# Kernel optimization log

Measured on AMD Instinct MI355X. Metric: run time of the kernel, lower is better.

Reference implementation:

```python
import jax, jax.numpy as jnp
import numpy as np

# Mamba hyperparams derived from DRMamba.__init__: d_model=dim=96, d_state=16, d_conv=4, expand=2
D_MODEL = 96
D_INNER = 192          # expand * d_model
D_STATE = 16
D_CONV = 4
DT_RANK = 6            # ceil(d_model / 16)
REVERSE = True


def setup_inputs() -> dict:
    key = jax.random.key(0)
    ks = jax.random.split(key, 8)
    s = lambda k, shape: jax.random.normal(k, shape, jnp.float32) * 0.02
    x = jax.random.normal(ks[0], (8, 96, 64, 64), jnp.float32)
    in_proj_w = s(ks[1], (2 * D_INNER, D_MODEL))
    conv_w = s(ks[2], (D_INNER, 1, D_CONV))            # depthwise conv kernel (O, I/groups=1, K)
    conv_b = jnp.zeros((D_INNER,), jnp.float32)
    x_proj_w = s(ks[3], (DT_RANK + 2 * D_STATE, D_INNER))
    dt_proj_w = s(ks[4], (D_INNER, DT_RANK))
    dt_proj_b = s(ks[5], (D_INNER,))
    # S4D-real init, as in standard Mamba
    A_log = jnp.log(jnp.broadcast_to(jnp.arange(1, D_STATE + 1, dtype=jnp.float32), (D_INNER, D_STATE)))
    D = jnp.ones((D_INNER,), jnp.float32)
    out_proj_w = s(ks[6], (D_MODEL, D_INNER))
    return dict(x=x, in_proj_w=in_proj_w, conv_w=conv_w, conv_b=conv_b,
                x_proj_w=x_proj_w, dt_proj_w=dt_proj_w, dt_proj_b=dt_proj_b,
                A_log=A_log, D=D, out_proj_w=out_proj_w)


def reference(x, in_proj_w, conv_w, conv_b, x_proj_w, dt_proj_w, dt_proj_b, A_log, D, out_proj_w):
    b, c, h, w = x.shape
    xs = jnp.flip(x, 1) if REVERSE else x
    seq = xs.reshape(b, c, h * w).transpose(0, 2, 1)              # (b, l, d_model)
    xz = seq @ in_proj_w.T                                        # (b, l, 2*d_inner)
    u, res = jnp.split(xz, 2, axis=-1)
    # causal depthwise conv1d over sequence (torch: padding=d_conv-1 then truncate to l)
    uc = jax.lax.conv_general_dilated(
        u.transpose(0, 2, 1), conv_w, (1,), [(D_CONV - 1, 0)],
        dimension_numbers=('NCH', 'OIH', 'NCH'), feature_group_count=D_INNER)
    uc = uc + conv_b[None, :, None]
    u = jax.nn.silu(uc.transpose(0, 2, 1))                        # (b, l, d_inner)
    # input-dependent SSM parameters
    dbc = u @ x_proj_w.T                                          # (b, l, dt_rank + 2*d_state)
    dt, B, C = jnp.split(dbc, [DT_RANK, DT_RANK + D_STATE], axis=-1)
    delta = jax.nn.softplus(dt @ dt_proj_w.T + dt_proj_b)         # (b, l, d_inner)
    A = -jnp.exp(A_log)                                           # (d_inner, d_state)
    dA = jnp.exp(jnp.einsum('bld,dn->bldn', delta, A))            # discretized A
    dBu = jnp.einsum('bld,bln,bld->bldn', delta, B, u)            # discretized B * u

    def step(state, inp):
        dA_t, dBu_t, C_t = inp                                    # (b,d,n), (b,d,n), (b,n)
        state = dA_t * state + dBu_t
        y_t = jnp.einsum('bdn,bn->bd', state, C_t)
        return state, y_t

    init = jnp.zeros((b, D_INNER, D_STATE), u.dtype)
    _, ys = jax.lax.scan(step, init,
                         (dA.transpose(1, 0, 2, 3), dBu.transpose(1, 0, 2, 3), C.transpose(1, 0, 2)))
    y = ys.transpose(1, 0, 2) + u * D                             # (b, l, d_inner)
    y = y * jax.nn.silu(res)
    out = y @ out_proj_w.T                                        # (b, l, d_model)
    out = out.transpose(0, 2, 1).reshape(b, c, h, w)
    return jnp.flip(out, 1) if REVERSE else out
```

## Files before the change

kernel.cpp:

```cpp
#include <hip/hip_runtime.h>
#include <math.h>

#define NBATCH 8
#define SEQL   4096
#define DMODEL 96
#define DINNER 192
#define DSTATE 16
#define NDBC   38
#define NCHUNK 128
#define CSTEP  32

__device__ __forceinline__ float siluf(float x) {
    return x / (1.f + expf(-x));
}
__device__ __forceinline__ float softplusf(float x) {
    return (x > 20.f) ? x : log1pf(expf(x));
}

__global__ __launch_bounds__(128) void k_in_proj(const float* __restrict__ x,
                                                 const float* __restrict__ w,
                                                 float* __restrict__ u_raw,
                                                 float* __restrict__ res)
{
    __shared__ float As[32][128];
    __shared__ float Wt[32][68];
    const int tid = threadIdx.x;
    const int jg = tid & 7;
    const int lg = tid >> 3;
    const int b = blockIdx.z;
    const int l0 = blockIdx.x * 128;
    const int jb = blockIdx.y * 64;

    float acc[8][8];
#pragma unroll
    for (int r = 0; r < 8; r++)
#pragma unroll
        for (int c = 0; c < 8; c++) acc[r][c] = 0.f;

    for (int kb = 0; kb < 3; kb++) {
        {
            const int ll4 = tid & 31;
            const int m0 = tid >> 5;
#pragma unroll
            for (int i = 0; i < 8; i++) {
                const int m = m0 + 4 * i;
                const float4 v = *reinterpret_cast<const float4*>(
                    &x[((size_t)b * 96 + (95 - (kb * 32 + m))) * 4096 + l0 + ll4 * 4]);
                *reinterpret_cast<float4*>(&As[m][ll4 * 4]) = v;
            }
        }
        {
            const int k4 = tid & 7;
            const int jl0 = tid >> 3;
#pragma unroll
            for (int i = 0; i < 4; i++) {
                const int jl = jl0 + 16 * i;
                const float4 v = *reinterpret_cast<const float4*>(
                    &w[(size_t)(jb + jl) * 96 + kb * 32 + k4 * 4]);
                Wt[k4 * 4 + 0][jl] = v.x;
                Wt[k4 * 4 + 1][jl] = v.y;
                Wt[k4 * 4 + 2][jl] = v.z;
                Wt[k4 * 4 + 3][jl] = v.w;
            }
        }
        __syncthreads();
#pragma unroll
        for (int k = 0; k < 32; k++) {
            const float4 a0 = *reinterpret_cast<const float4*>(&As[k][lg * 8]);
            const float4 a1 = *reinterpret_cast<const float4*>(&As[k][lg * 8 + 4]);
            const float4 w0 = *reinterpret_cast<const float4*>(&Wt[k][jg * 8]);
            const float4 w1 = *reinterpret_cast<const float4*>(&Wt[k][jg * 8 + 4]);
            const float av[8] = {a0.x, a0.y, a0.z, a0.w, a1.x, a1.y, a1.z, a1.w};
            const float wv[8] = {w0.x, w0.y, w0.z, w0.w, w1.x, w1.y, w1.z, w1.w};
#pragma unroll
            for (int r = 0; r < 8; r++)
#pragma unroll
                for (int c = 0; c < 8; c++) acc[r][c] = fmaf(av[r], wv[c], acc[r][c]);
        }
        __syncthreads();
    }

    float* outp;
    int col0;
    if (jb < 192) { outp = u_raw; col0 = jb + jg * 8; }
    else          { outp = res;   col0 = jb - 192 + jg * 8; }
#pragma unroll
    for (int r = 0; r < 8; r++) {
        const int row = l0 + lg * 8 + r;
        float* rowp = &outp[((size_t)b * 4096 + row) * 192 + col0];
        *reinterpret_cast<float4*>(rowp) =
            make_float4(acc[r][0], acc[r][1], acc[r][2], acc[r][3]);
        *reinterpret_cast<float4*>(rowp + 4) =
            make_float4(acc[r][4], acc[r][5], acc[r][6], acc[r][7]);
    }
}

__global__ __launch_bounds__(256) void k_xproj(const float* __restrict__ u_raw,
                                               const float* __restrict__ w,
                                               const float* __restrict__ cw,
                                               const float* __restrict__ cb,
                                               float* __restrict__ u,
                                               float* __restrict__ dbc,
                                               float* __restrict__ Barr,
                                               float* __restrict__ Carr)
{
    __shared__ float Ur[67][33];
    __shared__ float Us[64][36];
    __shared__ float Ws[64 * 32];
    const int tid = threadIdx.x, tx = tid & 15, ty = tid >> 4;
    const int b = blockIdx.y;
    const int l0 = blockIdx.x * 64;

    float acc[4][4];
#pragma unroll
    for (int r = 0; r < 4; r++)
#pragma unroll
        for (int c = 0; c < 4; c++) acc[r][c] = 0.f;

    const int ch = tid & 31;
    const int lblk = tid >> 5;

    for (int kb = 0; kb < 6; kb++) {
        for (int idx = tid; idx < 536; idx += 256) {
            const int row = idx >> 3;
            const int c4 = idx & 7;
            const int gl = l0 - 3 + row;
            float4 v = make_float4(0.f, 0.f, 0.f, 0.f);
            if (gl >= 0)
                v = *reinterpret_cast<const float4*>(
                    &u_raw[((size_t)b * 4096 + gl) * 192 + kb * 32 + c4 * 4]);
            Ur[row][c4 * 4 + 0] = v.x;
            Ur[row][c4 * 4 + 1] = v.y;
            Ur[row][c4 * 4 + 2] = v.z;
            Ur[row][c4 * 4 + 3] = v.w;
        }
        {
            const int k4 = tid & 7;
            const int jb0 = tid >> 3;
#pragma unroll
            for (int i = 0; i < 2; i++) {
                const int jl = jb0 + 32 * i;
                float4 v = make_float4(0.f, 0.f, 0.f, 0.f);
                if (jl < NDBC)
                    v = *reinterpret_cast<const float4*>(&w[(size_t)jl * 192 + kb * 32 + k4 * 4]);
                *reinterpret_cast<float4*>(
                    &Ws[jl * 32 + ((k4 ^ ((jl >> 2) & 7)) << 2)]) = v;
            }
        }
        __syncthreads();

        {
            const float4 wc = *reinterpret_cast<const float4*>(&cw[(kb * 32 + ch) * 4]);
            const float bias = cb[kb * 32 + ch];
#pragma unroll
            for (int r = 0; r < 8; r++) {
                const int l = lblk * 8 + r;
                float s = bias;
                s = fmaf(wc.x, Ur[l + 0][ch], s);
                s = fmaf(wc.y, Ur[l + 1][ch], s);
                s = fmaf(wc.z, Ur[l + 2][ch], s);
                s = fmaf(wc.w, Ur[l + 3][ch], s);
                Us[l][ch] = siluf(s);
            }
        }
        __syncthreads();

        for (int idx = tid; idx < 512; idx += 256) {
            const int row = idx >> 3;
            const int c4 = idx & 7;
            const float4 v = *reinterpret_cast<const float4*>(&Us[row][c4 * 4]);
            *reinterpret_cast<float4*>(
                &u[((size_t)b * 4096 + l0 + row) * 192 + kb * 32 + c4 * 4]) = v;
        }

        const int sw = tx & 7;
#pragma unroll
        for (int k4 = 0; k4 < 8; k4++) {
            float4 a4[4];
#pragma unroll
            for (int r = 0; r < 4; r++)
                a4[r] = *reinterpret_cast<const float4*>(&Us[ty * 4 + r][k4 * 4]);
            float4 w4[4];
#pragma unroll
            for (int c = 0; c < 4; c++)
                w4[c] = *reinterpret_cast<const float4*>(
                    &Ws[(tx * 4 + c) * 32 + ((k4 ^ sw) << 2)]);
#pragma unroll
            for (int r = 0; r < 4; r++)
#pragma unroll
                for (int c = 0; c < 4; c++) {
                    acc[r][c] = fmaf(a4[r].x, w4[c].x, acc[r][c]);
                    acc[r][c] = fmaf(a4[r].y, w4[c].y, acc[r][c]);
                    acc[r][c] = fmaf(a4[r].z, w4[c].z, acc[r][c]);
                    acc[r][c] = fmaf(a4[r].w, w4[c].w, acc[r][c]);
                }
        }
        __syncthreads();
    }

#pragma unroll
    for (int r = 0; r < 4; r++) {
        const size_t row = (size_t)b * 4096 + l0 + ty * 4 + r;
#pragma unroll
        for (int c = 0; c < 4; c++) {
            const int j = tx * 4 + c;
            if (j < 6)       dbc[row * NDBC + j] = acc[r][c];
            else if (j < 22) Barr[row * 16 + (j - 6)] = acc[r][c];
            else if (j < 38) Carr[row * 16 + (j - 22)] = acc[r][c];
        }
    }
}

__global__ __launch_bounds__(768) void k_dtproj(const float* __restrict__ dbc,
                                                const float* __restrict__ w,
                                                const float* __restrict__ bias,
                                                float* __restrict__ delta)
{
    const int j = threadIdx.x;
    const int row = blockIdx.x * 4 + threadIdx.y;
    const int b = blockIdx.y;
    const size_t g = (size_t)b * 4096 + row;
    const float* dr = &dbc[g * NDBC];
    float s = bias[j];
#pragma unroll
    for (int k = 0; k < 6; k++) s = fmaf(dr[k], w[j * 6 + k], s);
    delta[g * 192 + j] = softplusf(s);
}

__global__ __launch_bounds__(192) void k_scan1(const float* __restrict__ delta,
                                               const float* __restrict__ u,
                                               const float* __restrict__ Barr,
                                               const float* __restrict__ A_log,
                                               float* __restrict__ P,
                                               float* __restrict__ S)
{
    const int d = threadIdx.x;
    const int c = blockIdx.x;
    const int b = blockIdx.y;

    float a[16];
    {
        const float4* al = reinterpret_cast<const float4*>(&A_log[d * 16]);
#pragma unroll
        for (int i = 0; i < 4; i++) {
            const float4 v = al[i];
            a[4 * i + 0] = -expf(v.x);
            a[4 * i + 1] = -expf(v.y);
            a[4 * i + 2] = -expf(v.z);
            a[4 * i + 3] = -expf(v.w);
        }
    }
    float st[16], p[16];
#pragma unroll
    for (int n = 0; n < 16; n++) { st[n] = 0.f; p[n] = 1.f; }

    const size_t g0 = (size_t)b * 4096 + (size_t)c * CSTEP;
    const float* dp = delta + g0 * 192 + d;
    const float* up = u + g0 * 192 + d;
    const float* bp = Barr + g0 * 16;

#pragma unroll 2
    for (int t = 0; t < CSTEP; t++) {
        const float dt = dp[t * 192];
        const float dtu = dt * up[t * 192];
        float Bv[16];
        {
            const float4* b4 = reinterpret_cast<const float4*>(bp + t * 16);
#pragma unroll
            for (int i = 0; i < 4; i++) {
                const float4 v = b4[i];
                Bv[4 * i + 0] = v.x; Bv[4 * i + 1] = v.y;
                Bv[4 * i + 2] = v.z; Bv[4 * i + 3] = v.w;
            }
        }
#pragma unroll
        for (int n = 0; n < 16; n++) {
            const float dA = __expf(dt * a[n]);
            p[n] *= dA;
            st[n] = fmaf(dA, st[n], dtu * Bv[n]);
        }
    }

    const size_t idx = (((size_t)b * NCHUNK + c) * 192 + d) * 16;
    float4* Pp = reinterpret_cast<float4*>(&P[idx]);
    float4* Sp = reinterpret_cast<float4*>(&S[idx]);
#pragma unroll
    for (int i = 0; i < 4; i++) {
        Pp[i] = make_float4(p[4 * i], p[4 * i + 1], p[4 * i + 2], p[4 * i + 3]);
        Sp[i] = make_float4(st[4 * i], st[4 * i + 1], st[4 * i + 2], st[4 * i + 3]);
    }
}

__global__ __launch_bounds__(256) void k_scan2(const float* __restrict__ P,
                                               float* __restrict__ S)
{
    const int dn = blockIdx.x * 256 + threadIdx.x;
    const int b = blockIdx.y;
    float carry = 0.f;
    const size_t base = (size_t)b * NCHUNK * 3072 + dn;
#pragma unroll 8
    for (int c = 0; c < NCHUNK; c++) {
        const size_t idx = base + (size_t)c * 3072;
        const float p = P[idx];
        const float s = S[idx];
        S[idx] = carry;
        carry = fmaf(p, carry, s);
    }
}

__global__ __launch_bounds__(192) void k_scan3(const float* __restrict__ delta,
                                               const float* __restrict__ u,
                                               const float* __restrict__ Barr,
                                               const float* __restrict__ Carr,
                                               const float* __restrict__ A_log,
                                               const float* __restrict__ S,
                                               const float* __restrict__ Dp,
                                               const float* __restrict__ res,
                                               float* __restrict__ y)
{
    const int d = threadIdx.x;
    const int c = blockIdx.x;
    const int b = blockIdx.y;

    float a[16];
    {
        const float4* al = reinterpret_cast<const float4*>(&A_log[d * 16]);
#pragma unroll
        for (int i = 0; i < 4; i++) {
            const float4 v = al[i];
            a[4 * i + 0] = -expf(v.x);
            a[4 * i + 1] = -expf(v.y);
            a[4 * i + 2] = -expf(v.z);
            a[4 * i + 3] = -expf(v.w);
        }
    }
    float st[16];
    {
        const float4* Sp = reinterpret_cast<const float4*>(
            &S[(((size_t)b * NCHUNK + c) * 192 + d) * 16]);
#pragma unroll
        for (int i = 0; i < 4; i++) {
            const float4 v = Sp[i];
            st[4 * i + 0] = v.x; st[4 * i + 1] = v.y;
            st[4 * i + 2] = v.z; st[4 * i + 3] = v.w;
        }
    }
    const float Dd = Dp[d];

    const size_t g0 = (size_t)b * 4096 + (size_t)c * CSTEP;
    const float* dp = delta + g0 * 192 + d;
    const float* up = u + g0 * 192 + d;
    const float* rp = res + g0 * 192 + d;
    float* yp = y + g0 * 192 + d;
    const float* bp = Barr + g0 * 16;
    const float* cp = Carr + g0 * 16;

#pragma unroll 2
    for (int t = 0; t < CSTEP; t++) {
        const float dt = dp[t * 192];
        const float ut = up[t * 192];
        const float dtu = dt * ut;
        float Bv[16], Cv[16];
        {
            const float4* b4 = reinterpret_cast<const float4*>(bp + t * 16);
            const float4* c4 = reinterpret_cast<const float4*>(cp + t * 16);
#pragma unroll
            for (int i = 0; i < 4; i++) {
                const float4 v = b4[i];
                Bv[4 * i + 0] = v.x; Bv[4 * i + 1] = v.y;
                Bv[4 * i + 2] = v.z; Bv[4 * i + 3] = v.w;
                const float4 w = c4[i];
                Cv[4 * i + 0] = w.x; Cv[4 * i + 1] = w.y;
                Cv[4 * i + 2] = w.z; Cv[4 * i + 3] = w.w;
            }
        }
        float yt = 0.f;
#pragma unroll
        for (int n = 0; n < 16; n++) {
            const float dA = __expf(dt * a[n]);
            st[n] = fmaf(dA, st[n], dtu * Bv[n]);
            yt = fmaf(st[n], Cv[n], yt);
        }
        const float r = rp[t * 192];
        const float sig = __builtin_amdgcn_rcpf(1.f + __expf(-r));
        yp[t * 192] = fmaf(ut, Dd, yt) * (r * sig);
    }
}

__global__ __launch_bounds__(256) void k_outproj(const float* __restrict__ y,
                                                 const float* __restrict__ w,
                                                 float* __restrict__ out)
{
    __shared__ float Ws[64 * 32];
    const int tid = threadIdx.x, tx = tid & 15, ty = tid >> 4;
    const int b = blockIdx.z;
    const int l0 = blockIdx.x * 128;
    const int jb = blockIdx.y * 64;

    float acc[8][4];
#pragma unroll
    for (int r = 0; r < 8; r++)
#pragma unroll
        for (int c = 0; c < 4; c++) acc[r][c] = 0.f;

    for (int kb = 0; kb < 6; kb++) {
        {
            const int k4 = tid & 7;
            const int jb0 = tid >> 3;
#pragma unroll
            for (int i = 0; i < 2; i++) {
                const int jl = jb0 + 32 * i;
                const int j = jb + jl;
                float4 v = make_float4(0.f, 0.f, 0.f, 0.f);
                if (j < 96)
                    v = *reinterpret_cast<const float4*>(&w[(size_t)j * 192 + kb * 32 + k4 * 4]);
                *reinterpret_cast<float4*>(
                    &Ws[jl * 32 + ((k4 ^ ((jl >> 2) & 7)) << 2)]) = v;
            }
        }
        __syncthreads();
        const int sw = tx & 7;
#pragma unroll
        for (int k4 = 0; k4 < 8; k4++) {
            float4 a4[8];
#pragma unroll
            for (int r = 0; r < 8; r++) {
                const int row = l0 + ty * 8 + r;
                a4[r] = *reinterpret_cast<const float4*>(
                    &y[((size_t)b * 4096 + row) * 192 + kb * 32 + k4 * 4]);
            }
            float4 w4[4];
#pragma unroll
            for (int c = 0; c < 4; c++)
                w4[c] = *reinterpret_cast<const float4*>(
                    &Ws[(tx * 4 + c) * 32 + ((k4 ^ sw) << 2)]);
#pragma unroll
            for (int r = 0; r < 8; r++)
#pragma unroll
                for (int c = 0; c < 4; c++) {
                    acc[r][c] = fmaf(a4[r].x, w4[c].x, acc[r][c]);
                    acc[r][c] = fmaf(a4[r].y, w4[c].y, acc[r][c]);
                    acc[r][c] = fmaf(a4[r].z, w4[c].z, acc[r][c]);
                    acc[r][c] = fmaf(a4[r].w, w4[c].w, acc[r][c]);
                }
        }
        __syncthreads();
    }
#pragma unroll
    for (int c = 0; c < 4; c++) {
        const int j = jb + tx * 4 + c;
        if (j < 96) {
            const int ch = 95 - j;
            const float4 v0 = make_float4(acc[0][c], acc[1][c], acc[2][c], acc[3][c]);
            const float4 v1 = make_float4(acc[4][c], acc[5][c], acc[6][c], acc[7][c]);
            const size_t base = ((size_t)b * 96 + ch) * 4096 + l0 + ty * 8;
            *reinterpret_cast<float4*>(&out[base]) = v0;
            *reinterpret_cast<float4*>(&out[base + 4]) = v1;
        }
    }
}

extern "C" void kernel_launch(void* const* d_in, const int* in_sizes, int n_in,
                              void* d_out, int out_size, void* d_ws, size_t ws_size,
                              hipStream_t stream)
{
    const float* x       = (const float*)d_in[0];
    const float* in_w    = (const float*)d_in[1];
    const float* conv_w  = (const float*)d_in[2];
    const float* conv_b  = (const float*)d_in[3];
    const float* xproj_w = (const float*)d_in[4];
    const float* dt_w    = (const float*)d_in[5];
    const float* dt_b    = (const float*)d_in[6];
    const float* A_log   = (const float*)d_in[7];
    const float* Dp      = (const float*)d_in[8];
    const float* out_w   = (const float*)d_in[9];

    float* ws    = (float*)d_ws;
    float* u_raw = ws;
    float* res   = u_raw + 6291456;
    float* u     = res   + 6291456;
    float* delta = u     + 6291456;
    float* dbc   = delta + 6291456;
    float* Barr  = dbc   + 1245184;
    float* Carr  = Barr  + 524288;
    float* P     = Carr  + 524288;
    float* S     = P     + 3145728;
    float* yfin  = u_raw;

    hipLaunchKernelGGL(k_in_proj, dim3(32, 6, 8), dim3(128), 0, stream, x, in_w, u_raw, res);
    hipLaunchKernelGGL(k_xproj,   dim3(64, 8),    dim3(256), 0, stream,
                       u_raw, xproj_w, conv_w, conv_b, u, dbc, Barr, Carr);
    hipLaunchKernelGGL(k_dtproj,  dim3(1024, 8),  dim3(192, 4), 0, stream, dbc, dt_w, dt_b, delta);
    hipLaunchKernelGGL(k_scan1,   dim3(NCHUNK, 8), dim3(192), 0, stream, delta, u, Barr, A_log, P, S);
    hipLaunchKernelGGL(k_scan2,   dim3(12, 8),    dim3(256), 0, stream, P, S);
    hipLaunchKernelGGL(k_scan3,   dim3(NCHUNK, 8), dim3(192), 0, stream, delta, u, Barr, Carr, A_log, S, Dp, res, yfin);
    hipLaunchKernelGGL(k_outproj, dim3(32, 2, 8), dim3(256), 0, stream, yfin, out_w, (float*)d_out);
}
```

Before: 280.0 us.

## Recompute conv/silu and dt projection inside scan kernels, drop delta and u buffers

Removes the separate dt-projection kernel and stops writing the conv+silu output u and the full delta tensor to global memory. Both scan passes now recompute the causal depthwise conv, silu, the rank-6 dt projection and softplus from u_raw and a compact 8-wide dt array, trading extra ALU work for less HBM traffic. The in_proj GEMM is retiled to 256 threads with 128-column tiles, and fast intrinsic silu/softplus replace the libm versions, which slightly changes numerics.

After: 274.0 us. 2.1% less time.

```diff
diff --git a/kernel.cpp b/kernel.cpp
--- a/kernel.cpp
+++ b/kernel.cpp
@@ -13,23 +13,26 @@
 __device__ __forceinline__ float siluf(float x) {
     return x / (1.f + expf(-x));
 }
-__device__ __forceinline__ float softplusf(float x) {
-    return (x > 20.f) ? x : log1pf(expf(x));
-}
-
-__global__ __launch_bounds__(128) void k_in_proj(const float* __restrict__ x,
+__device__ __forceinline__ float silu_fast(float x) {
+    return x * __builtin_amdgcn_rcpf(1.f + __expf(-x));
+}
+__device__ __forceinline__ float softplus_fast(float x) {
+    return (x > 15.f) ? x : __logf(1.f + __expf(x));
+}
+
+__global__ __launch_bounds__(256) void k_in_proj(const float* __restrict__ x,
                                                  const float* __restrict__ w,
                                                  float* __restrict__ u_raw,
                                                  float* __restrict__ res)
 {
     __shared__ float As[32][128];
-    __shared__ float Wt[32][68];
+    __shared__ float Wt[32][133];
     const int tid = threadIdx.x;
-    const int jg = tid & 7;
-    const int lg = tid >> 3;
+    const int jg = tid & 15;
+    const int lg = tid >> 4;
     const int b = blockIdx.z;
     const int l0 = blockIdx.x * 128;
-    const int jb = blockIdx.y * 64;
+    const int jb = blockIdx.y * 128;
 
     float acc[8][8];
 #pragma unroll
@@ -42,8 +45,8 @@
             const int ll4 = tid & 31;
             const int m0 = tid >> 5;
 #pragma unroll
-            for (int i = 0; i < 8; i++) {
-                const int m = m0 + 4 * i;
+            for (int i = 0; i < 4; i++) {
+                const int m = m0 + 8 * i;
                 const float4 v = *reinterpret_cast<const float4*>(
                     &x[((size_t)b * 96 + (95 - (kb * 32 + m))) * 4096 + l0 + ll4 * 4]);
                 *reinterpret_cast<float4*>(&As[m][ll4 * 4]) = v;
@@ -54,7 +57,7 @@
             const int jl0 = tid >> 3;
 #pragma unroll
             for (int i = 0; i < 4; i++) {
-                const int jl = jl0 + 16 * i;
+                const int jl = jl0 + 32 * i;
                 const float4 v = *reinterpret_cast<const float4*>(
                     &w[(size_t)(jb + jl) * 96 + kb * 32 + k4 * 4]);
                 Wt[k4 * 4 + 0][jl] = v.x;
@@ -80,10 +83,11 @@
         __syncthreads();
     }
 
+    const int j0 = jb + jg * 8;
     float* outp;
     int col0;
-    if (jb < 192) { outp = u_raw; col0 = jb + jg * 8; }
-    else          { outp = res;   col0 = jb - 192 + jg * 8; }
+    if (j0 < 192) { outp = u_raw; col0 = j0; }
+    else          { outp = res;   col0 = j0 - 192; }
 #pragma unroll
     for (int r = 0; r < 8; r++) {
         const int row = l0 + lg * 8 + r;
@@ -99,8 +103,7 @@
                                                const float* __restrict__ w,
                                                const float* __restrict__ cw,
                                                const float* __restrict__ cb,
-                                               float* __restrict__ u,
-                                               float* __restrict__ dbc,
+                                               float* __restrict__ dtarr,
                                                float* __restrict__ Barr,
                                                float* __restrict__ Carr)
 {
@@ -165,14 +168,6 @@
         }
         __syncthreads();
 
-        for (int idx = tid; idx < 512; idx += 256) {
-            const int row = idx >> 3;
-            const int c4 = idx & 7;
-            const float4 v = *reinterpret_cast<const float4*>(&Us[row][c4 * 4]);
-            *reinterpret_cast<float4*>(
-                &u[((size_t)b * 4096 + l0 + row) * 192 + kb * 32 + c4 * 4]) = v;
-        }
-
         const int sw = tx & 7;
 #pragma unroll
         for (int k4 = 0; k4 < 8; k4++) {
@@ -204,33 +199,21 @@
 #pragma unroll
         for (int c = 0; c < 4; c++) {
             const int j = tx * 4 + c;
-            if (j < 6)       dbc[row * NDBC + j] = acc[r][c];
+            if (j < 6)       dtarr[row * 8 + j] = acc[r][c];
             else if (j < 22) Barr[row * 16 + (j - 6)] = acc[r][c];
             else if (j < 38) Carr[row * 16 + (j - 22)] = acc[r][c];
         }
     }
 }
 
-__global__ __launch_bounds__(768) void k_dtproj(const float* __restrict__ dbc,
-                                                const float* __restrict__ w,
-                                                const float* __restrict__ bias,
-                                                float* __restrict__ delta)
-{
-    const int j = threadIdx.x;
-    const int row = blockIdx.x * 4 + threadIdx.y;
-    const int b = blockIdx.y;
-    const size_t g = (size_t)b * 4096 + row;
-    const float* dr = &dbc[g * NDBC];
-    float s = bias[j];
-#pragma unroll
-    for (int k = 0; k < 6; k++) s = fmaf(dr[k], w[j * 6 + k], s);
-    delta[g * 192 + j] = softplusf(s);
-}
-
-__global__ __launch_bounds__(192) void k_scan1(const float* __restrict__ delta,
-                                               const float* __restrict__ u,
+__global__ __launch_bounds__(192) void k_scan1(const float* __restrict__ u_raw,
+                                               const float* __restrict__ dtarr,
                                                const float* __restrict__ Barr,
                                                const float* __restrict__ A_log,
+                                               const float* __restrict__ dt_w,
+                                               const float* __restrict__ dt_b,
+                                               const float* __restrict__ cw,
+                                               const float* __restrict__ cb,
                                                float* __restrict__ P,
                                                float* __restrict__ S)
 {
@@ -250,19 +233,50 @@
             a[4 * i + 3] = -expf(v.w);
         }
     }
+    float dw[6];
+#pragma unroll
+    for (int k = 0; k < 6; k++) dw[k] = dt_w[d * 6 + k];
+    const float db = dt_b[d];
+    const float4 wc = *reinterpret_cast<const float4*>(&cw[d * 4]);
+    const float cbias = cb[d];
+
     float st[16], p[16];
 #pragma unroll
     for (int n = 0; n < 16; n++) { st[n] = 0.f; p[n] = 1.f; }
 
-    const size_t g0 = (size_t)b * 4096 + (size_t)c * CSTEP;
-    const float* dp = delta + g0 * 192 + d;
-    const float* up = u + g0 * 192 + d;
+    const int t0 = c * CSTEP;
+    const size_t g0 = (size_t)b * 4096 + t0;
+    const float* up = u_raw + g0 * 192 + d;
+    const float* dtp = dtarr + g0 * 8;
     const float* bp = Barr + g0 * 16;
+
+    float w0 = 0.f, w1 = 0.f, w2 = 0.f;
+    if (t0 >= 3) {
+        w0 = up[-3 * 192];
+        w1 = up[-2 * 192];
+        w2 = up[-1 * 192];
+    }
 
 #pragma unroll 2
     for (int t = 0; t < CSTEP; t++) {
-        const float dt = dp[t * 192];
-        const float dtu = dt * up[t * 192];
+        const float w3 = up[t * 192];
+        float uc = cbias;
+        uc = fmaf(wc.x, w0, uc);
+        uc = fmaf(wc.y, w1, uc);
+        uc = fmaf(wc.z, w2, uc);
+        uc = fmaf(wc.w, w3, uc);
+        w0 = w1; w1 = w2; w2 = w3;
+        const float ut = silu_fast(uc);
+
+        const float4 q0 = *reinterpret_cast<const float4*>(dtp + t * 8);
+        const float4 q1 = *reinterpret_cast<const float4*>(dtp + t * 8 + 4);
+        float s = db;
+        s = fmaf(q0.x, dw[0], s); s = fmaf(q0.y, dw[1], s);
+        s = fmaf(q0.z, dw[2], s); s = fmaf(q0.w, dw[3], s);
+        s = fmaf(q1.x, dw[4], s); s = fmaf(q1.y, dw[5], s);
+        const float dt = softplus_fast(s);
+        const float dtu = dt * ut;
+
         float Bv[16];
         {
             const float4* b4 = reinterpret_cast<const float4*>(bp + t * 16);
@@ -308,11 +322,15 @@
     }
 }
 
-__global__ __launch_bounds__(192) void k_scan3(const float* __restrict__ delta,
-                                               const float* __restrict__ u,
+__global__ __launch_bounds__(192) void k_scan3(const float* __restrict__ u_raw,
+                                               const float* __restrict__ dtarr,
                                                const float* __restrict__ Barr,
                                                const float* __restrict__ Carr,
                                                const float* __restrict__ A_log,
+                                               const float* __restrict__ dt_w,
+                                               const float* __restrict__ dt_b,
+                                               const float* __restrict__ cw,
+                                               const float* __restrict__ cb,
                                                const float* __restrict__ S,
                                                const float* __restrict__ Dp,
                                                const float* __restrict__ res,
@@ -334,6 +352,14 @@
             a[4 * i + 3] = -expf(v.w);
         }
     }
+    float dw[6];
+#pragma unroll
+    for (int k = 0; k < 6; k++) dw[k] = dt_w[d * 6 + k];
+    const float db = dt_b[d];
+    const float4 wc = *reinterpret_cast<const float4*>(&cw[d * 4]);
+    const float cbias = cb[d];
+    const float Dd = Dp[d];
+
     float st[16];
     {
         const float4* Sp = reinterpret_cast<const float4*>(
@@ -345,21 +371,43 @@
             st[4 * i + 2] = v.z; st[4 * i + 3] = v.w;
         }
     }
-    const float Dd = Dp[d];
-
-    const size_t g0 = (size_t)b * 4096 + (size_t)c * CSTEP;
-    const float* dp = delta + g0 * 192 + d;
-    const float* up = u + g0 * 192 + d;
+
+    const int t0 = c * CSTEP;
+    const size_t g0 = (size_t)b * 4096 + t0;
+    const float* up = u_raw + g0 * 192 + d;
     const float* rp = res + g0 * 192 + d;
     float* yp = y + g0 * 192 + d;
+    const float* dtp = dtarr + g0 * 8;
     const float* bp = Barr + g0 * 16;
     const float* cp = Carr + g0 * 16;
 
+    float w0 = 0.f, w1 = 0.f, w2 = 0.f;
+    if (t0 >= 3) {
+        w0 = up[-3 * 192];
+        w1 = up[-2 * 192];
+        w2 = up[-1 * 192];
+    }
+
 #pragma unroll 2
     for (int t = 0; t < CSTEP; t++) {
-        const float dt = dp[t * 192];
-        const float ut = up[t * 192];
+        const float w3 = up[t * 192];
+        float uc = cbias;
+        uc = fmaf(wc.x, w0, uc);
+        uc = fmaf(wc.y, w1, uc);
+        uc = fmaf(wc.z, w2, uc);
+        uc = fmaf(wc.w, w3, uc);
+        w0 = w1; w1 = w2; w2 = w3;
+        const float ut = silu_fast(uc);
+
+        const float4 q0 = *reinterpret_cast<const float4*>(dtp + t * 8);
+        const float4 q1 = *reinterpret_cast<const float4*>(dtp + t * 8 + 4);
+        float s = db;
+        s = fmaf(q0.x, dw[0], s); s = fmaf(q0.y, dw[1], s);
+        s = fmaf(q0.z, dw[2], s); s = fmaf(q0.w, dw[3], s);
+        s = fmaf(q1.x, dw[4], s); s = fmaf(q1.y, dw[5], s);
+        const float dt = softplus_fast(s);
         const float dtu = dt * ut;
+
         float Bv[16], Cv[16];
         {
             const float4* b4 = reinterpret_cast<const float4*>(bp + t * 16);
@@ -382,8 +430,7 @@
             yt = fmaf(st[n], Cv[n], yt);
         }
         const float r = rp[t * 192];
-        const float sig = __builtin_amdgcn_rcpf(1.f + __expf(-r));
-        yp[t * 192] = fmaf(ut, Dd, yt) * (r * sig);
+        yp[t * 192] = fmaf(ut, Dd, yt) * silu_fast(r);
     }
 }
 
@@ -478,21 +525,21 @@
     float* ws    = (float*)d_ws;
     float* u_raw = ws;
     float* res   = u_raw + 6291456;
-    float* u     = res   + 6291456;
-    float* delta = u     + 6291456;
-    float* dbc   = delta + 6291456;
-    float* Barr  = dbc   + 1245184;
+    float* yfin  = res   + 6291456;
+    float* dtarr = yfin  + 6291456;
+    float* Barr  = dtarr + 262144;
     float* Carr  = Barr  + 524288;
     float* P     = Carr  + 524288;
     float* S     = P     + 3145728;
-    float* yfin  = u_raw;
-
-    hipLaunchKernelGGL(k_in_proj, dim3(32, 6, 8), dim3(128), 0, stream, x, in_w, u_raw, res);
+
+    hipLaunchKernelGGL(k_in_proj, dim3(32, 3, 8), dim3(256), 0, stream, x, in_w, u_raw, res);
     hipLaunchKernelGGL(k_xproj,   dim3(64, 8),    dim3(256), 0, stream,
-                       u_raw, xproj_w, conv_w, conv_b, u, dbc, Barr, Carr);
-    hipLaunchKernelGGL(k_dtproj,  dim3(1024, 8),  dim3(192, 4), 0, stream, dbc, dt_w, dt_b, delta);
-    hipLaunchKernelGGL(k_scan1,   dim3(NCHUNK, 8), dim3(192), 0, stream, delta, u, Barr, A_log, P, S);
+                       u_raw, xproj_w, conv_w, conv_b, dtarr, Barr, Carr);
+    hipLaunchKernelGGL(k_scan1,   dim3(NCHUNK, 8), dim3(192), 0, stream,
+                       u_raw, dtarr, Barr, A_log, dt_w, dt_b, conv_w, conv_b, P, S);
     hipLaunchKernelGGL(k_scan2,   dim3(12, 8),    dim3(256), 0, stream, P, S);
-    hipLaunchKernelGGL(k_scan3,   dim3(NCHUNK, 8), dim3(192), 0, stream, delta, u, Barr, Carr, A_log, S, Dp, res, yfin);
+    hipLaunchKernelGGL(k_scan3,   dim3(NCHUNK, 8), dim3(192), 0, stream,
+                       u_raw, dtarr, Barr, Carr, A_log, dt_w, dt_b, conv_w, conv_b,
+                       S, Dp, res, yfin);
     hipLaunchKernelGGL(k_outproj, dim3(32, 2, 8), dim3(256), 0, stream, yfin, out_w, (float*)d_out);
 }
```
